# Kernel tuning notes

Measured on AMD Instinct MI355X. Metric: run time of the kernel, lower is better.

Reference implementation:

```python
import jax, jax.numpy as jnp
import numpy as np

N, E, G = 10000, 80000, 32
Z, C, B, H = 10, 128, 8, 64
R_MAX = 5.0
AVG_NEIGH = 16.0
L_OFF = [0, 1, 4, 9, 16]  # slice offsets for l = 0..3 blocks of the SH vector


def real_sh(u):
    # Real spherical harmonics up to l=3, 'component' normalization (sum_m Y_lm^2 = 2l+1)
    x, y, z = u[:, 0], u[:, 1], u[:, 2]
    s3, s5, s15 = 3.0 ** 0.5, 5.0 ** 0.5, 15.0 ** 0.5
    cols = [
        jnp.ones_like(x),
        s3 * x, s3 * y, s3 * z,
        s15 * x * y, s15 * y * z, (s5 / 2) * (3 * z ** 2 - 1),
        s15 * x * z, (s15 / 2) * (x ** 2 - y ** 2),
        (70.0 ** 0.5 / 4) * (3 * x ** 2 * y - y ** 3),
        105.0 ** 0.5 * x * y * z,
        (42.0 ** 0.5 / 4) * y * (5 * z ** 2 - 1),
        (7.0 ** 0.5 / 2) * (5 * z ** 3 - 3 * z),
        (42.0 ** 0.5 / 4) * x * (5 * z ** 2 - 1),
        (105.0 ** 0.5 / 2) * z * (x ** 2 - y ** 2),
        (70.0 ** 0.5 / 4) * (x ** 3 - 3 * x * y ** 2),
    ]
    return jnp.stack(cols, axis=-1)  # [E, 16]


def poly_cutoff(x, p=5):
    f = (1.0 - (p + 1) * (p + 2) / 2 * x ** p
         + p * (p + 2) * x ** (p + 1)
         - p * (p + 1) / 2 * x ** (p + 2))
    return f * (x < 1.0).astype(f.dtype)


def setup_inputs() -> dict:
    key = jax.random.key(0)
    ks = jax.random.split(key, 20)
    vectors = jax.random.normal(ks[0], (E, 3), dtype=jnp.float32) * 1.5
    elem = jax.random.randint(ks[1], (N,), 0, Z)
    node_attrs = jax.nn.one_hot(elem, Z, dtype=jnp.float32)
    edge_index = jax.random.randint(ks[2], (2, E), 0, N).astype(jnp.int64)
    batch = jnp.sort(jax.random.randint(ks[3], (N,), 0, G)).astype(jnp.int64)

    def init(k, shape, fan_in):
        return jax.random.normal(k, shape, dtype=jnp.float32) / np.sqrt(fan_in)

    return {
        "vectors": vectors,
        "node_attrs": node_attrs,
        "W_embed": init(ks[4], (Z, C), Z),
        "atomic_energies": -jnp.arange(1, Z + 1, dtype=jnp.float32),
        "rw1": init(ks[5], (2, B, H), B),
        "rw2": init(ks[6], (2, H, H), H),
        "rw3": init(ks[7], (2, H, H), H),
        "rw4": init(ks[8], (2, H, 4 * C), H),
        "Wmix": init(ks[9], (2, 4, C, C), C),
        "U": init(ks[10], (2, Z, 4), Z),
        "Wprod": init(ks[11], (2, C, C), C),
        "Wsc": init(ks[12], (2, C, C), C),
        "Wro0": init(ks[13], (C, 1), C),
        "Wro1a": init(ks[14], (C, 16), C),
        "Wro1b": init(ks[15], (16, 1), 16),
        "scale": jnp.array([1.0], dtype=jnp.float32),
        "shift": jnp.array([0.0], dtype=jnp.float32),
        "edge_index": edge_index,
        "batch": batch,
    }


def reference(vectors, node_attrs, W_embed, atomic_energies, rw1, rw2, rw3, rw4,
              Wmix, U, Wprod, Wsc, Wro0, Wro1a, Wro1b, scale, shift,
              edge_index, batch):
    sender, receiver = edge_index[0], edge_index[1]
    r = jnp.linalg.norm(vectors, axis=-1)                     # [E]
    u = vectors / r[:, None]
    Y = real_sh(u)                                            # [E, 16]
    n = jnp.arange(1, B + 1, dtype=vectors.dtype)
    bessel = jnp.sqrt(2.0 / R_MAX) * jnp.sin(n[None] * jnp.pi * r[:, None] / R_MAX) / r[:, None]
    edge_feats = bessel * poly_cutoff(r / R_MAX)[:, None]     # [E, B]

    h = node_attrs @ W_embed                                  # [N, C] node embedding
    node_e0 = node_attrs @ atomic_energies                    # [N] atomic reference energies
    e0 = jax.ops.segment_sum(node_e0, batch, num_segments=G)  # [G]

    node_inter = jnp.zeros((node_attrs.shape[0],), dtype=vectors.dtype)
    for i in range(2):  # interaction layers (fixed small count)
        f = jax.nn.silu(edge_feats @ rw1[i])
        f = jax.nn.silu(f @ rw2[i])
        f = jax.nn.silu(f @ rw3[i])
        R_w = (f @ rw4[i]).reshape(-1, 4, C)                  # [E, 4, C] radial weights per l-path
        hs = h[sender]                                        # [E, C] edge gather
        A_parts = []
        for l in range(4):
            # channelwise tensor product (uvu): scalar node feats x Y_l -> l
            m = (R_w[:, l, :] * hs)[:, :, None] * Y[:, None, L_OFF[l]:L_OFF[l + 1]]  # [E, C, 2l+1]
            agg = jax.ops.segment_sum(m, receiver, num_segments=node_attrs.shape[0]) / AVG_NEIGH
            A_parts.append(jnp.einsum('ncm,cd->ndm', agg, Wmix[i, l]))
        # product basis: rotation-invariant powers per l, element-dependent contraction
        inv = jnp.stack([(p ** 2).sum(-1) for p in A_parts], axis=-1)  # [N, C, 4]
        w = node_attrs @ U[i]                                          # [N, 4]
        h = jnp.einsum('ncl,nl->nc', inv, w) @ Wprod[i] + h @ Wsc[i]   # product + residual sc
        if i == 0:
            node_inter = node_inter + (h @ Wro0)[:, 0]                 # linear readout
        else:
            node_inter = node_inter + (jax.nn.silu(h @ Wro1a) @ Wro1b)[:, 0]  # nonlinear readout
    node_inter = scale[0] * node_inter + shift[0]                       # scale-shift
    total = e0 + jax.ops.segment_sum(node_inter, batch, num_segments=G)
    return total  # [G] per-graph energies
```

## Files before the change

kernel.cpp:

```cpp
#include <hip/hip_runtime.h>
#include <hip/hip_fp8.h>

#define NN 10000
#define NE 80000
#define NG 32
#define NZ 10
#define NC 128
#define RMAXF 5.0f

typedef _Float16 f16;
typedef _Float16 half8 __attribute__((ext_vector_type(8)));
typedef float f32x4 __attribute__((ext_vector_type(4)));

#if defined(__has_builtin)
#if __has_builtin(__builtin_amdgcn_cvt_pk_fp8_f32) && __has_builtin(__builtin_amdgcn_cvt_f32_fp8)
#define HW_FP8 1
#endif
#endif

__device__ __forceinline__ float silu_f(float x) {
    return x / (1.0f + __expf(-x));
}

__device__ __forceinline__ int clampi(int v, int lo, int hi) {
    return v < lo ? lo : (v > hi ? hi : v);
}

__device__ __forceinline__ uint4 pack8f(float4 a, float4 b) {
    union { f16 h[8]; uint4 u; } P;
    P.h[0] = (f16)a.x; P.h[1] = (f16)a.y; P.h[2] = (f16)a.z; P.h[3] = (f16)a.w;
    P.h[4] = (f16)b.x; P.h[5] = (f16)b.y; P.h[6] = (f16)b.z; P.h[7] = (f16)b.w;
    return P.u;
}

__device__ __forceinline__ uint2 cvt8_fp8(uint4 v) {
    union { uint4 u; f16 h[8]; } I; I.u = v;
#ifdef HW_FP8
    int lo = 0, hi = 0;
    lo = __builtin_amdgcn_cvt_pk_fp8_f32((float)I.h[0], (float)I.h[1], lo, false);
    lo = __builtin_amdgcn_cvt_pk_fp8_f32((float)I.h[2], (float)I.h[3], lo, true);
    hi = __builtin_amdgcn_cvt_pk_fp8_f32((float)I.h[4], (float)I.h[5], hi, false);
    hi = __builtin_amdgcn_cvt_pk_fp8_f32((float)I.h[6], (float)I.h[7], hi, true);
    uint2 r; r.x = (unsigned)lo; r.y = (unsigned)hi; return r;
#else
    union { unsigned char b[8]; uint2 u2; } O;
#pragma unroll
    for (int j = 0; j < 8; j++) {
        __hip_fp8_e4m3 t((float)I.h[j]);
        O.b[j] = t.__x;
    }
    return O.u2;
#endif
}

__device__ __forceinline__ float fp8_to_f(unsigned char b) {
#ifdef HW_FP8
    return __builtin_amdgcn_cvt_f32_fp8((int)b, 0);
#else
    __hip_fp8_e4m3 t; t.__x = b;
    return (float)t;
#endif
}

__global__ void zero_stuff(int* counts, int* cursor, float* out) {
    int i = blockIdx.x * blockDim.x + threadIdx.x;
    if (i < NN) { counts[i] = 0; cursor[i] = 0; }
    if (i < NG) out[i] = 0.0f;
}

__global__ void prep_weights(const float* __restrict__ Wmix, const float* __restrict__ Wprod,
                             const float* __restrict__ Wsc,
                             const float* __restrict__ rw2, const float* __restrict__ rw3,
                             const float* __restrict__ rw4,
                             f16* __restrict__ WmixT, f16* __restrict__ WprodT, f16* __restrict__ WscT,
                             f16* __restrict__ w2T, f16* __restrict__ w3T, f16* __restrict__ w4T) {
    int i = blockIdx.x * blockDim.x + threadIdx.x;
    if (i < 2 * 4 * 128 * 128) {
        int cc = i & 127, d = (i >> 7) & 127, g = i >> 14;
        WmixT[i] = (f16)Wmix[((size_t)g * 128 + cc) * 128 + d];
    }
    if (i < 2 * 128 * 128) {
        int cc = i & 127, d = (i >> 7) & 127, g = i >> 14;
        WprodT[i] = (f16)Wprod[((size_t)g * 128 + cc) * 128 + d];
        WscT[i]   = (f16)Wsc[((size_t)g * 128 + cc) * 128 + d];
    }
    if (i < 2 * 512 * 64) {
        int k = i & 63, j = (i >> 6) & 511, ly = i >> 15;
        w4T[i] = (f16)rw4[((size_t)ly * 64 + k) * 512 + j];
    }
    if (i < 2 * 64 * 64) {
        int k = i & 63, j = (i >> 6) & 63, ly = i >> 12;
        w2T[i] = (f16)rw2[((size_t)ly * 64 + k) * 64 + j];
        w3T[i] = (f16)rw3[((size_t)ly * 64 + k) * 64 + j];
    }
}

__global__ void node_init(const float* __restrict__ attrs, const float* __restrict__ W_embed,
                          const float* __restrict__ ae, const float* __restrict__ U,
                          float* __restrict__ h, float* __restrict__ node_e0, float* __restrict__ wU) {
    int gid = blockIdx.x * blockDim.x + threadIdx.x;
    if (gid >= NN * NC) return;
    int n = gid >> 7, c = gid & 127;
    float a[NZ];
#pragma unroll
    for (int z = 0; z < NZ; z++) a[z] = attrs[n * NZ + z];
    float acc = 0.f;
#pragma unroll
    for (int z = 0; z < NZ; z++) acc += a[z] * W_embed[z * NC + c];
    h[(size_t)n * NC + c] = acc;
    if (c == 0) {
        float e = 0.f;
#pragma unroll
        for (int z = 0; z < NZ; z++) e += a[z] * ae[z];
        node_e0[n] = e;
    }
    if (c < 8) {
        int i = c >> 2, l = c & 3;
        float s = 0.f;
#pragma unroll
        for (int z = 0; z < NZ; z++) s += a[z] * U[i * NZ * 4 + z * 4 + l];
        wU[(size_t)i * NN * 4 + n * 4 + l] = s;
    }
}

__global__ void edge_geom(const float* __restrict__ vec, const int* __restrict__ elist,
                          float* __restrict__ Y2, float* __restrict__ ef2) {
    int i = blockIdx.x * blockDim.x + threadIdx.x;
    if (i >= NE) return;
    int e = clampi(elist[i], 0, NE - 1);
    float vx = vec[e * 3 + 0], vy = vec[e * 3 + 1], vz = vec[e * 3 + 2];
    float r = sqrtf(vx * vx + vy * vy + vz * vz);
    float inv = 1.0f / r;
    float x = vx * inv, y = vy * inv, z = vz * inv;
    const float s3 = 1.7320508075688772f;
    const float s5 = 2.23606797749979f;
    const float s15 = 3.872983346207417f;
    const float c9 = 2.091650066335189f;
    const float c10 = 10.246950765959598f;
    const float c11 = 1.6201851746019651f;
    const float c12 = 1.3228756555322954f;
    const float c14 = 5.123475382979799f;
    float o[16];
    o[0] = 1.0f;
    o[1] = s3 * x; o[2] = s3 * y; o[3] = s3 * z;
    o[4] = s15 * x * y; o[5] = s15 * y * z; o[6] = 0.5f * s5 * (3.f * z * z - 1.f);
    o[7] = s15 * x * z; o[8] = 0.5f * s15 * (x * x - y * y);
    o[9] = c9 * (3.f * x * x * y - y * y * y);
    o[10] = c10 * x * y * z;
    o[11] = c11 * y * (5.f * z * z - 1.f);
    o[12] = c12 * (5.f * z * z * z - 3.f * z);
    o[13] = c11 * x * (5.f * z * z - 1.f);
    o[14] = c14 * z * (x * x - y * y);
    o[15] = c9 * (x * x * x - 3.f * x * y * y);
#pragma unroll
    for (int m = 0; m < 16; m++) Y2[(size_t)i * 16 + m] = o[m];
    float xc = r / RMAXF;
    float cut = 0.0f;
    if (xc < 1.0f) {
        float x5 = xc * xc * xc * xc * xc;
        cut = 1.0f - 21.0f * x5 + 35.0f * x5 * xc - 15.0f * x5 * xc * xc;
    }
    float pref = sqrtf(2.0f / RMAXF) * inv * cut;
#pragma unroll
    for (int b = 0; b < 8; b++) {
        float arg = (float)(b + 1) * 3.14159265358979323846f * r / RMAXF;
        ef2[(size_t)i * 8 + b] = pref * sinf(arg);
    }
}

__global__ void hist_recv(const int* __restrict__ recv, int* __restrict__ counts) {
    int e = blockIdx.x * blockDim.x + threadIdx.x;
    if (e < NE) atomicAdd(&counts[clampi(recv[e], 0, NN - 1)], 1);
}

__global__ void scan_counts(const int* __restrict__ counts, int* __restrict__ rowstart) {
    __shared__ int part[1024];
    int t = threadIdx.x;
    const int CH = 10;
    int base = t * CH;
    int loc[CH];
    int s = 0;
#pragma unroll
    for (int j = 0; j < CH; j++) {
        int v = (base + j < NN) ? counts[base + j] : 0;
        loc[j] = s; s += v;
    }
    part[t] = s;
    __syncthreads();
    for (int off = 1; off < 1024; off <<= 1) {
        int v = (t >= off) ? part[t - off] : 0;
        __syncthreads();
        part[t] += v;
        __syncthreads();
    }
    int chunk = (t > 0) ? part[t - 1] : 0;
#pragma unroll
    for (int j = 0; j < CH; j++)
        if (base + j < NN) rowstart[base + j] = chunk + loc[j];
    if (t == 0) rowstart[NN] = part[1023];
}

__global__ void scatter_edges(const int* __restrict__ recv, const int* __restrict__ send,
                              const int* __restrict__ rowstart,
                              int* __restrict__ cursor, int* __restrict__ elist,
                              int* __restrict__ send2) {
    int e = blockIdx.x * blockDim.x + threadIdx.x;
    if (e < NE) {
        int r = clampi(recv[e], 0, NN - 1);
        int p = atomicAdd(&cursor[r], 1);
        int slot = clampi(rowstart[r] + p, 0, NE - 1);
        elist[slot] = e;
        send2[slot] = clampi(send[e], 0, NN - 1);
    }
}

__global__ __launch_bounds__(256) void edge_mlp(const float* __restrict__ ef2,
                                                const float* __restrict__ w1,
                                                const f16* __restrict__ w2T, const f16* __restrict__ w3T,
                                                const f16* __restrict__ w4T,
                                                unsigned char* __restrict__ Rw8) {
    __shared__ __align__(16) char L[16384];
    char* X1 = L;
    char* X2 = L + 8192;

    int tid = threadIdx.x;
    int lane = tid & 63;
    int w = tid >> 6;
    int ln = lane & 15, kq = lane >> 4;
    int eb = blockIdx.x * 64;

    {
        int jb = w * 16;
        const float4* efv = (const float4*)(ef2 + (size_t)(eb + lane) * 8);
        float4 ea = efv[0], eb4 = efv[1];
        float in8[8] = {ea.x, ea.y, ea.z, ea.w, eb4.x, eb4.y, eb4.z, eb4.w};
        f16 pk[16];
#pragma unroll
        for (int j = 0; j < 16; j++) {
            float a = 0.f;
#pragma unroll
            for (int b = 0; b < 8; b++) a += in8[b] * w1[b * 64 + jb + j];
            pk[j] = (f16)silu_f(a);
        }
        int base = lane * 128 + jb * 2;
#pragma unroll
        for (int t = 0; t < 2; t++) {
            int byte = (base + t * 16) ^ ((lane & 7) << 4);
            *(uint4*)(X1 + byte) = ((uint4*)pk)[t];
        }
    }
    __syncthreads();

    {
        half8 a[2];
#pragma unroll
        for (int kc = 0; kc < 2; kc++) {
            int row = w * 16 + ln;
            int byte = (row * 128 + kc * 64 + kq * 16) ^ ((row & 7) << 4);
            a[kc] = *(const half8*)(X1 + byte);
        }
#pragma unroll
        for (int nt = 0; nt < 4; nt++) {
            f32x4 acc = {0.f, 0.f, 0.f, 0.f};
#pragma unroll
            for (int kc = 0; kc < 2; kc++) {
                half8 b = *(const half8*)(w2T + (nt * 16 + ln) * 64 + kc * 32 + kq * 8);
                acc = __builtin_amdgcn_mfma_f32_16x16x32_f16(a[kc], b, acc, 0, 0, 0);
            }
#pragma unroll
            for (int r = 0; r < 4; r++) {
                int row = w * 16 + kq * 4 + r;
                int byte = (row * 128 + (nt * 16 + ln) * 2) ^ ((row & 7) << 4);
                *(f16*)(X2 + byte) = (f16)silu_f(acc[r]);
            }
        }
    }
    __syncthreads();

    {
        half8 a[2];
#pragma unroll
        for (int kc = 0; kc < 2; kc++) {
            int row = w * 16 + ln;
            int byte = (row * 128 + kc * 64 + kq * 16) ^ ((row & 7) << 4);
            a[kc] = *(const half8*)(X2 + byte);
        }
#pragma unroll
        for (int nt = 0; nt < 4; nt++) {
            f32x4 acc = {0.f, 0.f, 0.f, 0.f};
#pragma unroll
            for (int kc = 0; kc < 2; kc++) {
                half8 b = *(const half8*)(w3T + (nt * 16 + ln) * 64 + kc * 32 + kq * 8);
                acc = __builtin_amdgcn_mfma_f32_16x16x32_f16(a[kc], b, acc, 0, 0, 0);
            }
#pragma unroll
            for (int r = 0; r < 4; r++) {
                int row = w * 16 + kq * 4 + r;
                int byte = (row * 128 + (nt * 16 + ln) * 2) ^ ((row & 7) << 4);
                *(f16*)(X1 + byte) = (f16)silu_f(acc[r]);
            }
        }
    }
    __syncthreads();

    half8 a3[2];
#pragma unroll
    for (int kc = 0; kc < 2; kc++) {
        int row = w * 16 + ln;
        int byte = (row * 128 + kc * 64 + kq * 16) ^ ((row & 7) << 4);
        a3[kc] = *(const half8*)(X1 + byte);
    }
    for (int s = 0; s < 8; s++) {
#pragma unroll
        for (int nt = 0; nt < 4; nt++) {
            f32x4 acc = {0.f, 0.f, 0.f, 0.f};
#pragma unroll
            for (int kc = 0; kc < 2; kc++) {
                half8 b = *(const half8*)(w4T + (s * 64 + nt * 16 + ln) * 64 + kc * 32 + kq * 8);
                acc = __builtin_amdgcn_mfma_f32_16x16x32_f16(a3[kc], b, acc, 0, 0, 0);
            }
#pragma unroll
            for (int r = 0; r < 4; r++) {
                int row = w * 16 + kq * 4 + r;
                int byte = (row * 128 + (nt * 16 + ln) * 2) ^ ((row & 7) << 4);
                *(f16*)(X2 + byte) = (f16)acc[r];
            }
        }
        __syncthreads();
#pragma unroll
        for (int it = 0; it < 2; it++) {
            int i = it * 256 + tid;
            int row = i >> 3, chunk = i & 7;
            int byte = (row * 128 + chunk * 16) ^ ((row & 7) << 4);
            uint4 v = *(const uint4*)(X2 + byte);
            *(uint2*)(Rw8 + (size_t)(eb + row) * 512 + s * 64 + chunk * 8) = cvt8_fp8(v);
        }
        __syncthreads();
    }
}

__global__ __launch_bounds__(256) void agg_only(const int* __restrict__ rowstart,
                                                const int* __restrict__ send2, const float* __restrict__ h_in,
                                                const unsigned char* __restrict__ Rw8, const float* __restrict__ Y2,
                                                f16* __restrict__ aggH) {
    __shared__ int sL[64];
    int n = blockIdx.x, tid = threadIdx.x;
    int c = tid & 127, mh = tid >> 7;
    float acc[8];
#pragma unroll
    for (int q = 0; q < 8; q++) acc[q] = 0.f;
    int beg = rowstart[n], end = rowstart[n + 1];
    for (int base = beg; base < end; base += 64) {
        int cnt = min(64, end - base);
        __syncthreads();
        if (tid < cnt) sL[tid] = send2[base + tid];
        __syncthreads();
        for (int j = 0; j < cnt; j++) {
            int idx = base + j;
            int s = sL[j];
            float hs = h_in[(size_t)s * NC + c];
            const unsigned char* rwp = Rw8 + (size_t)idx * 512;
            const float4* yv = (const float4*)(Y2 + (size_t)idx * 16 + mh * 8);
            float4 ya = yv[0], yb = yv[1];
            float y[8] = {ya.x, ya.y, ya.z, ya.w, yb.x, yb.y, yb.z, yb.w};
            if (mh == 0) {
                float p0 = fp8_to_f(rwp[c]) * hs;
                float p1 = fp8_to_f(rwp[128 + c]) * hs;
                float p2 = fp8_to_f(rwp[256 + c]) * hs;
                acc[0] += p0 * y[0];
                acc[1] += p1 * y[1]; acc[2] += p1 * y[2]; acc[3] += p1 * y[3];
                acc[4] += p2 * y[4]; acc[5] += p2 * y[5]; acc[6] += p2 * y[6]; acc[7] += p2 * y[7];
            } else {
                float p2 = fp8_to_f(rwp[256 + c]) * hs;
                float p3 = fp8_to_f(rwp[384 + c]) * hs;
                acc[0] += p2 * y[0];
#pragma unroll
                for (int q = 1; q < 8; q++) acc[q] += p3 * y[q];
            }
        }
    }
    const float inv16 = 1.0f / 16.0f;
#pragma unroll
    for (int q = 0; q < 8; q++)
        aggH[(size_t)n * 2048 + (size_t)(mh * 8 + q) * NC + c] = (f16)(acc[q] * inv16);
}

__global__ __launch_bounds__(256) void mix_a(
    const f16* __restrict__ aggH, const f16* __restrict__ WmixT,
    const float* __restrict__ wU, f16* __restrict__ invwG, int layer)
{
    __shared__ __align__(16) char Lb[16384];

    int tid = threadIdx.x;
    int b = blockIdx.x;
    int nb = (b >> 1) * 16;
    int half = b & 1;
    int lane = tid & 63;
    int w = tid >> 6;
    int dt = half * 4 + w;
    int ln = lane & 15, kq = lane >> 4;
    char* myB = Lb + w * 4096;

    float4 wUreg[4];
#pragma unroll
    for (int r = 0; r < 4; r++)
        wUreg[r] = *(const float4*)(wU + (size_t)(nb + kq * 4 + r) * 4);

    float invwacc[4] = {0.f, 0.f, 0.f, 0.f};
    const f16* aggRow = aggH + (size_t)(nb + ln) * 2048 + kq * 8;

#pragma unroll
    for (int g = 0; g < 4; g++) {
        const int mstart = (g == 0) ? 0 : (g == 1) ? 1 : (g == 2) ? 4 : 9;
        const int mend   = (g == 0) ? 1 : (g == 1) ? 4 : (g == 2) ? 9 : 16;
        {
            const f16* Bt = WmixT + ((size_t)(layer * 4 + g) << 14);
#pragma unroll
            for (int i = 0; i < 4; i++) {
                int q = i * 64 + lane;
                int row = q >> 4, col = q & 15;
                uint4 v = *(const uint4*)(Bt + (dt * 16 + row) * 128 + col * 8);
                int byte = (row * 256 + col * 16) ^ ((row & 7) << 4);
                *(uint4*)(myB + byte) = v;
            }
        }
#pragma unroll
        for (int m = mstart; m < mend; m++) {
            f32x4 acc = {0.f, 0.f, 0.f, 0.f};
#pragma unroll
            for (int k = 0; k < 4; k++) {
                half8 a = *(const half8*)(aggRow + m * 128 + k * 32);
                int byte = (ln * 256 + k * 64 + kq * 16) ^ ((ln & 7) << 4);
                half8 bb = *(const half8*)(myB + byte);
                acc = __builtin_amdgcn_mfma_f32_16x16x32_f16(a, bb, acc, 0, 0, 0);
            }
#pragma unroll
            for (int r = 0; r < 4; r++) {
                float wur = (g == 0) ? wUreg[r].x : (g == 1) ? wUreg[r].y : (g == 2) ? wUreg[r].z : wUreg[r].w;
                invwacc[r] += acc[r] * acc[r] * wur;
            }
        }
    }

#pragma unroll
    for (int r = 0; r < 4; r++)
        invwG[(size_t)(nb + kq * 4 + r) * 128 + dt * 16 + ln] = (f16)invwacc[r];
}

__global__ __launch_bounds__(512) void mix_b(
    const f16* __restrict__ invwG, const float* __restrict__ h_in,
    const f16* __restrict__ WprodT, const f16* __restrict__ WscT,
    const float* __restrict__ Wro0, const float* __restrict__ Wro1a, const float* __restrict__ Wro1b,
    float* __restrict__ h_out, float* __restrict__ ni, int layer)
{
    __shared__ __align__(16) char Lb[13312];
    f16*   invwH = (f16*)(Lb);
    f16*   hH    = (f16*)(Lb + 4096);
    f16*   houtH = (f16*)(Lb + 8192);
    float* p16L  = (float*)(Lb + 12288);

    int tid = threadIdx.x;
    int nb = blockIdx.x * 16;
    int lane = tid & 63;
    int w = tid >> 6;
    int ln = lane & 15, kq = lane >> 4;

    if (tid < 256) {
        int node = tid >> 4, ch = tid & 15;
        int byte = (node * 256 + ch * 16) ^ ((node & 7) << 4);
        uint4 iv = *(const uint4*)(invwG + (size_t)(nb + node) * 128 + ch * 8);
        *(uint4*)((char*)invwH + byte) = iv;
        const float4* hp = (const float4*)(h_in + (size_t)(nb + node) * 128 + ch * 8);
        float4 g0 = hp[0], g1 = hp[1];
        *(uint4*)((char*)hH + byte) = pack8f(g0, g1);
    }
    __syncthreads();

    {
        half8 ai[4], ah[4];
#pragma unroll
        for (int k = 0; k < 4; k++) {
            int byte = (ln * 256 + (k * 32 + kq * 8) * 2) ^ ((ln & 7) << 4);
            ai[k] = *(const half8*)((char*)invwH + byte);
            ah[k] = *(const half8*)((char*)hH + byte);
        }
        const f16* Bp = WprodT + ((size_t)layer << 14);
        const f16* Bs = WscT + ((size_t)layer << 14);
        f32x4 acc = {0.f, 0.f, 0.f, 0.f};
#pragma unroll
        for (int k = 0; k < 4; k++) {
            half8 bb = *(const half8*)(Bp + (w * 16 + ln) * 128 + k * 32 + kq * 8);
            acc = __builtin_amdgcn_mfma_f32_16x16x32_f16(ai[k], bb, acc, 0, 0, 0);
        }
#pragma unroll
        for (int k = 0; k < 4; k++) {
            half8 bb = *(const half8*)(Bs + (w * 16 + ln) * 128 + k * 32 + kq * 8);
            acc = __builtin_amdgcn_mfma_f32_16x16x32_f16(ah[k], bb, acc, 0, 0, 0);
        }
#pragma unroll
        for (int r = 0; r < 4; r++) {
            int node = kq * 4 + r;
            int d = w * 16 + ln;
            h_out[(size_t)(nb + node) * 128 + d] = acc[r];
            houtH[node * 128 + d] = (f16)acc[r];
        }
    }
    __syncthreads();

    if (tid < 256) {
        int rn = tid >> 4, rj = tid & 15;
        if (layer == 0) {
            float s = 0.f;
            for (int cc = rj; cc < 128; cc += 16) s += (float)houtH[rn * 128 + cc] * Wro0[cc];
            p16L[tid] = s;
        } else {
            float s = 0.f;
            for (int cc = 0; cc < 128; cc++) s += (float)houtH[rn * 128 + cc] * Wro1a[cc * 16 + rj];
            s = silu_f(s);
            p16L[tid] = s * Wro1b[rj];
        }
    }
    __syncthreads();
    if (tid < 16) {
        float t = 0.f;
#pragma unroll
        for (int j = 0; j < 16; j++) t += p16L[tid * 16 + j];
        ni[nb + tid] = (layer == 0) ? t : (ni[nb + tid] + t);
    }
}

__global__ void finalize(const float* __restrict__ node_e0, const float* __restrict__ ni,
                         const int* __restrict__ batch, const float* __restrict__ scale,
                         const float* __restrict__ shift, float* __restrict__ out) {
    __shared__ float bins[NG];
    int tid = threadIdx.x;
    if (tid < NG) bins[tid] = 0.f;
    __syncthreads();
    int n = blockIdx.x * blockDim.x + tid;
    if (n < NN) {
        float v = node_e0[n] + scale[0] * ni[n] + shift[0];
        atomicAdd(&bins[clampi(batch[n], 0, NG - 1)], v);
    }
    __syncthreads();
    if (tid < NG) atomicAdd(&out[tid], bins[tid]);
}

extern "C" void kernel_launch(void* const* d_in, const int* in_sizes, int n_in,
                              void* d_out, int out_size, void* d_ws, size_t ws_size,
                              hipStream_t stream) {
    (void)in_sizes; (void)n_in; (void)out_size; (void)ws_size;
    const float* vectors = (const float*)d_in[0];
    const float* attrs   = (const float*)d_in[1];
    const float* W_embed = (const float*)d_in[2];
    const float* ae      = (const float*)d_in[3];
    const float* rw1     = (const float*)d_in[4];
    const float* rw2     = (const float*)d_in[5];
    const float* rw3     = (const float*)d_in[6];
    const float* rw4     = (const float*)d_in[7];
    const float* Wmix    = (const float*)d_in[8];
    const float* U       = (const float*)d_in[9];
    const float* Wprod   = (const float*)d_in[10];
    const float* Wsc     = (const float*)d_in[11];
    const float* Wro0    = (const float*)d_in[12];
    const float* Wro1a   = (const float*)d_in[13];
    const float* Wro1b   = (const float*)d_in[14];
    const float* scale   = (const float*)d_in[15];
    const float* shift   = (const float*)d_in[16];
    const int* eidx      = (const int*)d_in[17];
    const int* batch     = (const int*)d_in[18];
    float* out = (float*)d_out;

    char* w = (char*)d_ws;
    size_t off = 0;
    auto alloc = [&](size_t bytes) -> void* {
        void* p = (void*)(w + off);
        off += (bytes + 255) & ~(size_t)255;
        return p;
    };
    float* Y2      = (float*)alloc((size_t)NE * 16 * 4);
    float* ef2     = (float*)alloc((size_t)NE * 8 * 4);
    unsigned char* Rw8 = (unsigned char*)alloc((size_t)NE * 512);
    f16*   aggH    = (f16*)  alloc((size_t)NN * 2048 * 2);
    float* hA      = (float*)alloc((size_t)NN * NC * 4);
    float* hB      = (float*)alloc((size_t)NN * NC * 4);
    f16*   invwG   = (f16*)  alloc((size_t)NN * NC * 2);
    float* wU      = (float*)alloc((size_t)2 * NN * 4 * 4);
    float* node_e0 = (float*)alloc((size_t)NN * 4);
    float* ni      = (float*)alloc((size_t)NN * 4);
    f16*   WmixT   = (f16*)  alloc((size_t)2 * 4 * 128 * 128 * 2);
    f16*   WprodT  = (f16*)  alloc((size_t)2 * 128 * 128 * 2);
    f16*   WscT    = (f16*)  alloc((size_t)2 * 128 * 128 * 2);
    f16*   w2T     = (f16*)  alloc((size_t)2 * 64 * 64 * 2);
    f16*   w3T     = (f16*)  alloc((size_t)2 * 64 * 64 * 2);
    f16*   w4T     = (f16*)  alloc((size_t)2 * 512 * 64 * 2);
    int* counts    = (int*)alloc((size_t)NN * 4);
    int* rowstart  = (int*)alloc((size_t)(NN + 1) * 4);
    int* cursor    = (int*)alloc((size_t)NN * 4);
    int* elist     = (int*)alloc((size_t)NE * 4);
    int* send2     = (int*)alloc((size_t)NE * 4);

    const int* send = eidx;
    const int* recv = eidx + NE;
    zero_stuff<<<(NN + 255) / 256, 256, 0, stream>>>(counts, cursor, out);
    prep_weights<<<512, 256, 0, stream>>>(Wmix, Wprod, Wsc, rw2, rw3, rw4,
                                          WmixT, WprodT, WscT, w2T, w3T, w4T);
    node_init<<<(NN * NC + 255) / 256, 256, 0, stream>>>(attrs, W_embed, ae, U, hA, node_e0, wU);
    hist_recv<<<(NE + 255) / 256, 256, 0, stream>>>(recv, counts);
    scan_counts<<<1, 1024, 0, stream>>>(counts, rowstart);
    scatter_edges<<<(NE + 255) / 256, 256, 0, stream>>>(recv, send, rowstart, cursor, elist, send2);
    edge_geom<<<(NE + 255) / 256, 256, 0, stream>>>(vectors, elist, Y2, ef2);

    float* hcur = hA;
    float* hnext = hB;
    for (int layer = 0; layer < 2; layer++) {
        edge_mlp<<<NE / 64, 256, 0, stream>>>(
            ef2, rw1 + layer * 8 * 64,
            w2T + (size_t)layer * 64 * 64, w3T + (size_t)layer * 64 * 64,
            w4T + (size_t)layer * 512 * 64, Rw8);
        agg_only<<<NN, 256, 0, stream>>>(rowstart, send2, hcur, Rw8, Y2, aggH);
        mix_a<<<(NN / 16) * 2, 256, 0, stream>>>(
            aggH, WmixT, wU + (size_t)layer * NN * 4, invwG, layer);
        mix_b<<<NN / 16, 512, 0, stream>>>(
            invwG, hcur, WprodT, WscT, Wro0, Wro1a, Wro1b, hnext, ni, layer);
        float* t = hcur; hcur = hnext; hnext = t;
    }
    finalize<<<(NN + 255) / 256, 256, 0, stream>>>(node_e0, ni, batch, scale, shift, out);
}
```

Before: 333.3 us.

## Store radial weights transposed per 64-edge tile, write fp8 directly from MFMA

The radial MLP epilogue now packs the four MFMA accumulator rows straight to fp8 and writes them to a transposed per-block layout ([channel][edge] within each 64-edge tile). This drops the LDS staging buffer and two __syncthreads per output slice. The aggregation kernel reads this layout with stride-64 byte loads per channel, so adjacent threads' reads are spread 64 bytes apart instead of sitting next to each other. That likely hurts coalescing of the gather, which may offset the epilogue savings.

```diff
diff --git a/kernel.cpp b/kernel.cpp
--- a/kernel.cpp
+++ b/kernel.cpp
@@ -33,23 +33,19 @@
     return P.u;
 }
 
-__device__ __forceinline__ uint2 cvt8_fp8(uint4 v) {
-    union { uint4 u; f16 h[8]; } I; I.u = v;
+__device__ __forceinline__ unsigned int cvt4_fp8(float a0, float a1, float a2, float a3) {
 #ifdef HW_FP8
-    int lo = 0, hi = 0;
-    lo = __builtin_amdgcn_cvt_pk_fp8_f32((float)I.h[0], (float)I.h[1], lo, false);
-    lo = __builtin_amdgcn_cvt_pk_fp8_f32((float)I.h[2], (float)I.h[3], lo, true);
-    hi = __builtin_amdgcn_cvt_pk_fp8_f32((float)I.h[4], (float)I.h[5], hi, false);
-    hi = __builtin_amdgcn_cvt_pk_fp8_f32((float)I.h[6], (float)I.h[7], hi, true);
-    uint2 r; r.x = (unsigned)lo; r.y = (unsigned)hi; return r;
+    int lo = 0;
+    lo = __builtin_amdgcn_cvt_pk_fp8_f32(a0, a1, lo, false);
+    lo = __builtin_amdgcn_cvt_pk_fp8_f32(a2, a3, lo, true);
+    return (unsigned)lo;
 #else
-    union { unsigned char b[8]; uint2 u2; } O;
-#pragma unroll
-    for (int j = 0; j < 8; j++) {
-        __hip_fp8_e4m3 t((float)I.h[j]);
-        O.b[j] = t.__x;
-    }
-    return O.u2;
+    union { unsigned char b[4]; unsigned u; } O;
+    __hip_fp8_e4m3 t0(a0); O.b[0] = t0.__x;
+    __hip_fp8_e4m3 t1(a1); O.b[1] = t1.__x;
+    __hip_fp8_e4m3 t2(a2); O.b[2] = t2.__x;
+    __hip_fp8_e4m3 t3(a3); O.b[3] = t3.__x;
+    return O.u;
 #endif
 }
 
@@ -310,6 +306,8 @@
         int byte = (row * 128 + kc * 64 + kq * 16) ^ ((row & 7) << 4);
         a3[kc] = *(const half8*)(X1 + byte);
     }
+    unsigned char* outT = Rw8 + (size_t)blockIdx.x * 32768;
+    int erow = w * 16 + kq * 4;
     for (int s = 0; s < 8; s++) {
 #pragma unroll
         for (int nt = 0; nt < 4; nt++) {
@@ -319,23 +317,9 @@
                 half8 b = *(const half8*)(w4T + (s * 64 + nt * 16 + ln) * 64 + kc * 32 + kq * 8);
                 acc = __builtin_amdgcn_mfma_f32_16x16x32_f16(a3[kc], b, acc, 0, 0, 0);
             }
-#pragma unroll
-            for (int r = 0; r < 4; r++) {
-                int row = w * 16 + kq * 4 + r;
-                int byte = (row * 128 + (nt * 16 + ln) * 2) ^ ((row & 7) << 4);
-                *(f16*)(X2 + byte) = (f16)acc[r];
-            }
-        }
-        __syncthreads();
-#pragma unroll
-        for (int it = 0; it < 2; it++) {
-            int i = it * 256 + tid;
-            int row = i >> 3, chunk = i & 7;
-            int byte = (row * 128 + chunk * 16) ^ ((row & 7) << 4);
-            uint4 v = *(const uint4*)(X2 + byte);
-            *(uint2*)(Rw8 + (size_t)(eb + row) * 512 + s * 64 + chunk * 8) = cvt8_fp8(v);
-        }
-        __syncthreads();
+            unsigned int pk = cvt4_fp8(acc[0], acc[1], acc[2], acc[3]);
+            *(unsigned int*)(outT + (s * 64 + nt * 16 + ln) * 64 + erow) = pk;
+        }
     }
 }
 
@@ -359,20 +343,20 @@
             int idx = base + j;
             int s = sL[j];
             float hs = h_in[(size_t)s * NC + c];
-            const unsigned char* rwp = Rw8 + (size_t)idx * 512;
+            const unsigned char* rwt = Rw8 + (size_t)(idx >> 6) * 32768 + (idx & 63);
             const float4* yv = (const float4*)(Y2 + (size_t)idx * 16 + mh * 8);
             float4 ya = yv[0], yb = yv[1];
             float y[8] = {ya.x, ya.y, ya.z, ya.w, yb.x, yb.y, yb.z, yb.w};
             if (mh == 0) {
-                float p0 = fp8_to_f(rwp[c]) * hs;
-                float p1 = fp8_to_f(rwp[128 + c]) * hs;
-                float p2 = fp8_to_f(rwp[256 + c]) * hs;
+                float p0 = fp8_to_f(rwt[(size_t)c * 64]) * hs;
+                float p1 = fp8_to_f(rwt[(size_t)(128 + c) * 64]) * hs;
+                float p2 = fp8_to_f(rwt[(size_t)(256 + c) * 64]) * hs;
                 acc[0] += p0 * y[0];
                 acc[1] += p1 * y[1]; acc[2] += p1 * y[2]; acc[3] += p1 * y[3];
                 acc[4] += p2 * y[4]; acc[5] += p2 * y[5]; acc[6] += p2 * y[6]; acc[7] += p2 * y[7];
             } else {
-                float p2 = fp8_to_f(rwp[256 + c]) * hs;
-                float p3 = fp8_to_f(rwp[384 + c]) * hs;
+                float p2 = fp8_to_f(rwt[(size_t)(256 + c) * 64]) * hs;
+                float p3 = fp8_to_f(rwt[(size_t)(384 + c) * 64]) * hs;
                 acc[0] += p2 * y[0];
 #pragma unroll
                 for (int q = 1; q < 8; q++) acc[q] += p3 * y[q];
```

After: 555.1 us. 66.5% more time.
